# Kernel optimization log

Measured on AMD Instinct MI355X. Metric: run time of the kernel, lower is better.

## Reference

```python
import jax, jax.numpy as jnp
import numpy as np

TAU = 0.07
EPS = 1e-12  # F.normalize eps


def _l2norm(x):
    n = jnp.sqrt(jnp.sum(x * x, axis=-1, keepdims=True))
    return x / jnp.maximum(n, EPS)


def setup_inputs() -> dict:
    key = jax.random.key(0)
    k1, k2 = jax.random.split(key)
    n_e, e_dim = 4096, 64
    z = jax.random.normal(k1, (8, e_dim, 64, 64), dtype=jnp.float32)
    # embedding initialized uniform(-1/n_e, 1/n_e) in the module
    embedding = jax.random.uniform(k2, (n_e, e_dim), dtype=jnp.float32,
                                   minval=-1.0 / n_e, maxval=1.0 / n_e)
    return {"z": z, "embedding": embedding}


def reference(z, embedding):
    # z: [b, c, h, w] -> [b, h, w, c]
    b, c, h, w = z.shape
    z_bhwc = jnp.transpose(z.astype(jnp.float32), (0, 2, 3, 1))
    z_flat = _l2norm(z_bhwc.reshape(-1, c))          # [N, d]
    emb = _l2norm(embedding)                          # [n_e, d]
    logits = jnp.einsum('bd,nd->bn', z_flat, emb)     # [N, n_e]
    probs = jax.nn.softmax(logits / TAU, axis=-1)
    z_q_flat = probs @ emb                            # [N, d]
    z_q = _l2norm(z_q_flat.reshape(b, h, w, c))
    indices = jnp.argmax(probs, axis=-1)              # [N]
    entropy_loss = jnp.asarray(0.0, dtype=jnp.float32)  # eval mode
    z_q = jnp.transpose(z_q, (0, 3, 1, 2))            # back to [b, c, h, w]
    return (z_q, entropy_loss, indices)
```

## Files before the change

### kernel.cpp

```cpp
#include <hip/hip_runtime.h>
#include <hip/hip_bf16.h>

typedef unsigned short u16;
typedef unsigned int u32;
typedef __attribute__((ext_vector_type(4))) float f32x4;
typedef __attribute__((ext_vector_type(16))) float f32x16;
typedef __attribute__((ext_vector_type(4))) u32 u32x4;
typedef __attribute__((ext_vector_type(8))) __bf16 bf16x8;

#define LAM 20.60992915555662f

__device__ __forceinline__ void gl16(const void* g, void* l) {
  __builtin_amdgcn_global_load_lds(
      (const __attribute__((address_space(1))) unsigned int*)g,
      (__attribute__((address_space(3))) unsigned int*)l, 16, 0, 0);
}

__device__ __forceinline__ u32 cvtpk(float a, float b) {
  u32 r;
  asm("v_cvt_pk_bf16_f32 %0, %1, %2" : "=v"(r) : "v"(a), "v"(b));
  return r;
}

__device__ __forceinline__ float exp2a(float x) {
  float r;
  asm("v_exp_f32 %0, %1" : "=v"(r) : "v"(x));
  return r;
}

__global__ __launch_bounds__(256) void k_emb_prep(
    const float* __restrict__ emb, float* __restrict__ einv,
    u16* __restrict__ ehi, u16* __restrict__ elo, u16* __restrict__ et,
    float* __restrict__ out) {
  __shared__ u16 ehl[64][72];
  const int ch = blockIdx.x, t = threadIdx.x;
  const int e = t >> 2, q = t & 3;
  const int ge = ch * 64 + e;
  float v[16];
#pragma unroll
  for (int b = 0; b < 4; b++)
    *reinterpret_cast<float4*>(v + 4 * b) =
        *reinterpret_cast<const float4*>(emb + (size_t)ge * 64 + q * 16 + 4 * b);
  float ss = 0.f;
#pragma unroll
  for (int j = 0; j < 16; j++) ss += v[j] * v[j];
  ss += __shfl_xor(ss, 1);
  ss += __shfl_xor(ss, 2);
  float inv = 1.0f / fmaxf(sqrtf(ss), 1e-12f);
  if (q == 0) einv[ge] = inv;
  u16 hi[16], lo[16];
#pragma unroll
  for (int j = 0; j < 16; j++) {
    float n = v[j] * inv;
    __bf16 h = (__bf16)n;
    hi[j] = __builtin_bit_cast(u16, h);
    __bf16 l = (__bf16)(n - (float)h);
    lo[j] = __builtin_bit_cast(u16, l);
  }
#pragma unroll
  for (int bb = 0; bb < 2; bb++) {
    int b = 2 * q + bb;
    int pos = (b ^ (e & 7)) * 8;
    *reinterpret_cast<uint4*>(ehi + (size_t)ge * 64 + pos) =
        *reinterpret_cast<const uint4*>(hi + 8 * bb);
    *reinterpret_cast<uint4*>(elo + (size_t)ge * 64 + pos) =
        *reinterpret_cast<const uint4*>(lo + 8 * bb);
  }
  *reinterpret_cast<uint4*>(&ehl[e][q * 16]) = *reinterpret_cast<const uint4*>(hi);
  *reinterpret_cast<uint4*>(&ehl[e][q * 16 + 8]) = *reinterpret_cast<const uint4*>(hi + 8);
  __syncthreads();
  {
    const int d = t >> 2, eq = t & 3;
    u16 vals[16];
#pragma unroll
    for (int j = 0; j < 16; j++) vals[j] = ehl[eq * 16 + j][d];
#pragma unroll
    for (int bb = 0; bb < 2; bb++) {
      int b = 2 * eq + bb;
      int pos = (b ^ (d & 7)) * 8;
      *reinterpret_cast<uint4*>(et + (size_t)ch * 4096 + d * 64 + pos) =
          *reinterpret_cast<const uint4*>(vals + 8 * bb);
    }
  }
  if (ch == 0 && t == 0) out[2097152] = 0.0f;
}

__global__ __launch_bounds__(256) void k_z_prep(
    const float* __restrict__ z, u16* __restrict__ zhi, u16* __restrict__ zlo) {
  __shared__ float zt[64][65];
  int tid = threadIdx.x;
  int p0 = blockIdx.x * 64;
  const float* zb = z + (size_t)(p0 >> 12) * 262144 + (p0 & 4095);
#pragma unroll
  for (int k = 0; k < 4; k++) {
    int idx = k * 1024 + tid * 4;
    int c = idx >> 6, px = idx & 63;
    float4 v = *reinterpret_cast<const float4*>(zb + (size_t)c * 4096 + px);
    zt[c][px] = v.x; zt[c][px + 1] = v.y; zt[c][px + 2] = v.z; zt[c][px + 3] = v.w;
  }
  __syncthreads();
  int px = tid >> 2, cq = tid & 3;
  float ss = 0.f;
#pragma unroll
  for (int j = 0; j < 16; j++) { float v = zt[cq * 16 + j][px]; ss += v * v; }
  ss += __shfl_xor(ss, 1);
  ss += __shfl_xor(ss, 2);
  float inv = 1.0f / fmaxf(sqrtf(ss), 1e-12f);
  int p = p0 + px;
#pragma unroll
  for (int j0 = 0; j0 < 16; j0 += 4) {
    u16 hs[4], ls[4];
#pragma unroll
    for (int j = 0; j < 4; j++) {
      float n = zt[cq * 16 + j0 + j][px] * inv;
      __bf16 h = (__bf16)n;
      hs[j] = __builtin_bit_cast(u16, h);
      __bf16 l = (__bf16)(n - (float)h);
      ls[j] = __builtin_bit_cast(u16, l);
    }
    *reinterpret_cast<ushort4*>(zhi + (size_t)p * 64 + cq * 16 + j0) = make_ushort4(hs[0], hs[1], hs[2], hs[3]);
    *reinterpret_cast<ushort4*>(zlo + (size_t)p * 64 + cq * 16 + j0) = make_ushort4(ls[0], ls[1], ls[2], ls[3]);
  }
}

__global__ __launch_bounds__(256, 4) void k_main(
    const u16* __restrict__ zhi, const u16* __restrict__ zlo,
    const u16* __restrict__ ehi, const u16* __restrict__ elo,
    const u16* __restrict__ et, float* __restrict__ Osum,
    float* __restrict__ tv1, float* __restrict__ tv2, u32* __restrict__ tix) {
  __shared__ __align__(16) u16 sA[2][2][4096];
  __shared__ __align__(16) u16 sV[4096];
  const int t = threadIdx.x;
  const int w = t >> 6, lane = t & 63;
  const int H = lane >> 5, c = lane & 31;
  const int bx = blockIdx.x;
  const int s = bx >> 8, tile = bx & 255;
  const int px = tile * 128 + w * 32 + c;

  bf16x8 qh[4], ql[4];
#pragma unroll
  for (int kc = 0; kc < 4; kc++) {
    qh[kc] = *reinterpret_cast<const bf16x8*>(zhi + (size_t)px * 64 + kc * 16 + H * 8);
    ql[kc] = *reinterpret_cast<const bf16x8*>(zlo + (size_t)px * 64 + kc * 16 + H * 8);
  }

  int cb[4];
#pragma unroll
  for (int kc = 0; kc < 4; kc++) cb[kc] = 8 * ((2 * kc + H) ^ (c & 7));
  const int row0 = c * 64, row1 = (32 + c) * 64;

  f32x16 O0 = (f32x16)(0.0f), O1 = (f32x16)(0.0f);
  float v1 = -1e30f, v2 = -1e30f;
  int i1 = 0, i2 = 1;

  {
    const size_t gb = (size_t)(s * 16) * 4096;
#pragma unroll
    for (int u = 0; u < 2; u++) {
      int off = t * 8 + u * 2048;
      gl16(ehi + gb + off, &sA[0][0][off]);
      gl16(elo + gb + off, &sA[0][1][off]);
    }
  }
  __syncthreads();

  for (int ch = 0; ch < 16; ch++) {
    const int cur = ch & 1;
    {
      const size_t gv = (size_t)(s * 16 + ch) * 4096;
#pragma unroll
      for (int u = 0; u < 2; u++) {
        int off = t * 8 + u * 2048;
        gl16(et + gv + off, &sV[off]);
      }
    }
    if (ch + 1 < 16) {
      const size_t gb = (size_t)(s * 16 + ch + 1) * 4096;
#pragma unroll
      for (int u = 0; u < 2; u++) {
        int off = t * 8 + u * 2048;
        gl16(ehi + gb + off, &sA[cur ^ 1][0][off]);
        gl16(elo + gb + off, &sA[cur ^ 1][1][off]);
      }
    }
    const u16* sh = sA[cur][0];
    const u16* sl = sA[cur][1];

    f32x16 sa0, sa1;
    {
      f32x16 acc = (f32x16)(0.0f);
#pragma unroll
      for (int kc = 0; kc < 4; kc++) {
        bf16x8 ah = *reinterpret_cast<const bf16x8*>(&sh[row0 + cb[kc]]);
        bf16x8 al = *reinterpret_cast<const bf16x8*>(&sl[row0 + cb[kc]]);
        acc = __builtin_amdgcn_mfma_f32_32x32x16_bf16(ah, qh[kc], acc, 0, 0, 0);
        acc = __builtin_amdgcn_mfma_f32_32x32x16_bf16(al, qh[kc], acc, 0, 0, 0);
        acc = __builtin_amdgcn_mfma_f32_32x32x16_bf16(ah, ql[kc], acc, 0, 0, 0);
      }
      sa0 = acc;
    }
    {
      f32x16 acc = (f32x16)(0.0f);
#pragma unroll
      for (int kc = 0; kc < 4; kc++) {
        bf16x8 ah = *reinterpret_cast<const bf16x8*>(&sh[row1 + cb[kc]]);
        bf16x8 al = *reinterpret_cast<const bf16x8*>(&sl[row1 + cb[kc]]);
        acc = __builtin_amdgcn_mfma_f32_32x32x16_bf16(ah, qh[kc], acc, 0, 0, 0);
        acc = __builtin_amdgcn_mfma_f32_32x32x16_bf16(al, qh[kc], acc, 0, 0, 0);
        acc = __builtin_amdgcn_mfma_f32_32x32x16_bf16(ah, ql[kc], acc, 0, 0, 0);
      }
      sa1 = acc;
    }

    const int e0 = (s * 16 + ch) * 64;
    u32 pk[2][8], pko[2][8];
#pragma unroll
    for (int nt = 0; nt < 2; nt++) {
      float pe[16];
#pragma unroll
      for (int reg = 0; reg < 16; reg++) {
        float svv = nt ? sa1[reg] : sa0[reg];
        int eidx = e0 + nt * 32 + (reg & 3) + 8 * (reg >> 2) + 4 * H;
        if (svv > v1) { v2 = v1; i2 = i1; v1 = svv; i1 = eidx; }
        else if (svv > v2) { v2 = svv; i2 = eidx; }
        pe[reg] = exp2a(fmaf(svv, LAM, -LAM));
      }
#pragma unroll
      for (int qq = 0; qq < 8; qq++) pk[nt][qq] = cvtpk(pe[2 * qq], pe[2 * qq + 1]);
#pragma unroll
      for (int qq = 0; qq < 8; qq++) pko[nt][qq] = (u32)__shfl_xor((int)pk[nt][qq], 32);
    }

    __syncthreads();

#pragma unroll
    for (int km = 0; km < 4; km++) {
      const int nt = km >> 1, m1 = km & 1;
      u32x4 bv;
      bv.x = H ? pko[nt][(2 * m1 + 1) * 2 + 0] : pk[nt][(2 * m1) * 2 + 0];
      bv.y = H ? pko[nt][(2 * m1 + 1) * 2 + 1] : pk[nt][(2 * m1) * 2 + 1];
      bv.z = H ? pk[nt][(2 * m1 + 1) * 2 + 0] : pko[nt][(2 * m1) * 2 + 0];
      bv.w = H ? pk[nt][(2 * m1 + 1) * 2 + 1] : pko[nt][(2 * m1) * 2 + 1];
      bf16x8 pb = __builtin_bit_cast(bf16x8, bv);
      bf16x8 a0 = *reinterpret_cast<const bf16x8*>(&sV[row0 + cb[km]]);
      bf16x8 a1 = *reinterpret_cast<const bf16x8*>(&sV[row1 + cb[km]]);
      O0 = __builtin_amdgcn_mfma_f32_32x32x16_bf16(a0, pb, O0, 0, 0, 0);
      O1 = __builtin_amdgcn_mfma_f32_32x32x16_bf16(a1, pb, O1, 0, 0, 0);
    }
    __syncthreads();
  }

  {
    float o1 = __shfl_xor(v1, 32); int oi1 = __shfl_xor(i1, 32);
    float o2 = __shfl_xor(v2, 32); int oi2 = __shfl_xor(i2, 32);
    if (o1 > v1) { v2 = v1; i2 = i1; v1 = o1; i1 = oi1; }
    else if (o1 > v2) { v2 = o1; i2 = oi1; }
    if (o2 > v2) { v2 = o2; i2 = oi2; }
  }
  if (H == 0) {
    int o = s * 32768 + px;
    tv1[o] = v1;
    tv2[o] = v2;
    tix[o] = ((u32)i1 << 12) | (u32)i2;
  }
#pragma unroll
  for (int reg = 0; reg < 16; reg++) {
    int d0 = (reg & 3) + 8 * (reg >> 2) + 4 * H;
    unsafeAtomicAdd(&Osum[(size_t)d0 * 32768 + px], O0[reg]);
    unsafeAtomicAdd(&Osum[(size_t)(d0 + 32) * 32768 + px], O1[reg]);
  }
}

__global__ __launch_bounds__(256) void k_combine(
    const float* __restrict__ Osum, const float* __restrict__ tv1,
    const float* __restrict__ tv2, const u32* __restrict__ tix,
    const float* __restrict__ z, const float* __restrict__ emb,
    const float* __restrict__ einv, float* __restrict__ out) {
  const int t = threadIdx.x;
  const int px = blockIdx.x * 256 + t;
  const int b_ = px >> 12, hw = px & 4095;

  float ss = 0.f;
#pragma unroll 8
  for (int d = 0; d < 64; d++) {
    float v = Osum[(size_t)d * 32768 + px];
    ss = fmaf(v, v, ss);
  }
  float inv = 1.0f / fmaxf(sqrtf(ss), 1e-30f);
#pragma unroll 8
  for (int d = 0; d < 64; d++) {
    float v = Osum[(size_t)d * 32768 + px];
    out[(size_t)b_ * 262144 + (size_t)d * 4096 + hw] = v * inv;
  }

  float m1 = tv1[px], m2 = tv2[px];
  u32 ia = tix[px];
  int j1 = (int)(ia >> 12), j2 = (int)(ia & 0xFFF);
#pragma unroll
  for (int sg = 1; sg < 4; sg++) {
    float b1 = tv1[sg * 32768 + px], b2 = tv2[sg * 32768 + px];
    u32 ib = tix[sg * 32768 + px];
    int k1 = (int)(ib >> 12), k2 = (int)(ib & 0xFFF);
    if (b1 > m1) { m2 = m1; j2 = j1; m1 = b1; j1 = k1; }
    else if (b1 > m2) { m2 = b1; j2 = k1; }
    if (b2 > m2) { m2 = b2; j2 = k2; }
  }
  {
    const float* zc = z + (size_t)b_ * 262144 + hw;
    const float* e1 = emb + (size_t)j1 * 64;
    const float* e2 = emb + (size_t)j2 * 64;
    double d1 = 0.0, d2 = 0.0;
#pragma unroll 8
    for (int cc = 0; cc < 64; cc++) {
      double zv = (double)zc[(size_t)cc * 4096];
      d1 += zv * (double)e1[cc];
      d2 += zv * (double)e2[cc];
    }
    d1 *= (double)einv[j1];
    d2 *= (double)einv[j2];
    int best = (d2 > d1 || (d2 == d1 && j2 < j1)) ? j2 : j1;
    out[2097153 + px] = (float)best;
  }
}

extern "C" void kernel_launch(void* const* d_in, const int* in_sizes, int n_in,
                              void* d_out, int out_size, void* d_ws, size_t ws_size,
                              hipStream_t stream) {
  const float* z = (const float*)d_in[0];
  const float* emb = (const float*)d_in[1];
  float* out = (float*)d_out;
  char* ws = (char*)d_ws;
  float* Osum = (float*)(ws + 0);
  float* tv1  = (float*)(ws + 8388608);
  float* tv2  = (float*)(ws + 8912896);
  u32*   tix  = (u32*)(ws + 9437184);
  u16*   zhi  = (u16*)(ws + 9961472);
  u16*   zlo  = (u16*)(ws + 14155776);
  u16*   ehi  = (u16*)(ws + 18350080);
  u16*   elo  = (u16*)(ws + 18874368);
  u16*   et   = (u16*)(ws + 19398656);
  float* einv = (float*)(ws + 19922944);

  hipMemsetAsync(Osum, 0, 8388608, stream);
  k_emb_prep<<<dim3(64), dim3(256), 0, stream>>>(emb, einv, ehi, elo, et, out);
  k_z_prep<<<dim3(512), dim3(256), 0, stream>>>(z, zhi, zlo);
  k_main<<<dim3(1024), dim3(256), 0, stream>>>(zhi, zlo, ehi, elo, et, Osum, tv1, tv2, tix);
  k_combine<<<dim3(128), dim3(256), 0, stream>>>(Osum, tv1, tv2, tix, z, emb, einv, out);
}
```

Measured before the change: 180.9 us.

## Merge prep kernels, pack top-2 as integers, use permlane32 swap, widen combine

Fuses the embedding and z prep kernels into one launch that branches on block index. In the main kernel, the float top-2 tracking with index bookkeeping is replaced by packed fixed-point score|index u32 values updated with integer max/min. The cross-half shuffles used to assemble MFMA B operands are replaced by v_permlane32_swap. The combine kernel now gives four threads to each pixel, using 4x more blocks and shuffle reductions. The fixed-point quantization of scores (about 18 bits) can make near-ties order differently, though the fp64 recheck of the top two candidates reduces the effect on the final argmax.

```diff
diff --git a/kernel.cpp b/kernel.cpp
--- a/kernel.cpp
+++ b/kernel.cpp
@@ -28,98 +28,103 @@
   return r;
 }
 
-__global__ __launch_bounds__(256) void k_emb_prep(
-    const float* __restrict__ emb, float* __restrict__ einv,
-    u16* __restrict__ ehi, u16* __restrict__ elo, u16* __restrict__ et,
+__device__ __forceinline__ u32 umaxu(u32 a, u32 b) { return a > b ? a : b; }
+__device__ __forceinline__ u32 uminu(u32 a, u32 b) { return a < b ? a : b; }
+
+__global__ __launch_bounds__(256) void k_prep(
+    const float* __restrict__ emb, const float* __restrict__ z,
+    float* __restrict__ einv, u16* __restrict__ ehi, u16* __restrict__ elo,
+    u16* __restrict__ et, u16* __restrict__ zhi, u16* __restrict__ zlo,
     float* __restrict__ out) {
-  __shared__ u16 ehl[64][72];
-  const int ch = blockIdx.x, t = threadIdx.x;
-  const int e = t >> 2, q = t & 3;
-  const int ge = ch * 64 + e;
-  float v[16];
-#pragma unroll
-  for (int b = 0; b < 4; b++)
-    *reinterpret_cast<float4*>(v + 4 * b) =
-        *reinterpret_cast<const float4*>(emb + (size_t)ge * 64 + q * 16 + 4 * b);
-  float ss = 0.f;
-#pragma unroll
-  for (int j = 0; j < 16; j++) ss += v[j] * v[j];
-  ss += __shfl_xor(ss, 1);
-  ss += __shfl_xor(ss, 2);
-  float inv = 1.0f / fmaxf(sqrtf(ss), 1e-12f);
-  if (q == 0) einv[ge] = inv;
-  u16 hi[16], lo[16];
-#pragma unroll
-  for (int j = 0; j < 16; j++) {
-    float n = v[j] * inv;
-    __bf16 h = (__bf16)n;
-    hi[j] = __builtin_bit_cast(u16, h);
-    __bf16 l = (__bf16)(n - (float)h);
-    lo[j] = __builtin_bit_cast(u16, l);
-  }
-#pragma unroll
-  for (int bb = 0; bb < 2; bb++) {
-    int b = 2 * q + bb;
-    int pos = (b ^ (e & 7)) * 8;
-    *reinterpret_cast<uint4*>(ehi + (size_t)ge * 64 + pos) =
-        *reinterpret_cast<const uint4*>(hi + 8 * bb);
-    *reinterpret_cast<uint4*>(elo + (size_t)ge * 64 + pos) =
-        *reinterpret_cast<const uint4*>(lo + 8 * bb);
-  }
-  *reinterpret_cast<uint4*>(&ehl[e][q * 16]) = *reinterpret_cast<const uint4*>(hi);
-  *reinterpret_cast<uint4*>(&ehl[e][q * 16 + 8]) = *reinterpret_cast<const uint4*>(hi + 8);
-  __syncthreads();
-  {
-    const int d = t >> 2, eq = t & 3;
-    u16 vals[16];
-#pragma unroll
-    for (int j = 0; j < 16; j++) vals[j] = ehl[eq * 16 + j][d];
+  __shared__ union {
+    u16 ehl[64][72];
+    float zt[64][65];
+  } sm;
+  const int bx = blockIdx.x, t = threadIdx.x;
+  if (bx < 64) {
+    const int ch = bx;
+    const int e = t >> 2, q = t & 3;
+    const int ge = ch * 64 + e;
+    float v[16];
+#pragma unroll
+    for (int b = 0; b < 4; b++)
+      *reinterpret_cast<float4*>(v + 4 * b) =
+          *reinterpret_cast<const float4*>(emb + (size_t)ge * 64 + q * 16 + 4 * b);
+    float ss = 0.f;
+#pragma unroll
+    for (int j = 0; j < 16; j++) ss += v[j] * v[j];
+    ss += __shfl_xor(ss, 1);
+    ss += __shfl_xor(ss, 2);
+    float inv = 1.0f / fmaxf(sqrtf(ss), 1e-12f);
+    if (q == 0) einv[ge] = inv;
+    u16 hi[16], lo[16];
+#pragma unroll
+    for (int j = 0; j < 16; j++) {
+      float n = v[j] * inv;
+      __bf16 h = (__bf16)n;
+      hi[j] = __builtin_bit_cast(u16, h);
+      __bf16 l = (__bf16)(n - (float)h);
+      lo[j] = __builtin_bit_cast(u16, l);
+    }
 #pragma unroll
     for (int bb = 0; bb < 2; bb++) {
-      int b = 2 * eq + bb;
-      int pos = (b ^ (d & 7)) * 8;
-      *reinterpret_cast<uint4*>(et + (size_t)ch * 4096 + d * 64 + pos) =
-          *reinterpret_cast<const uint4*>(vals + 8 * bb);
-    }
-  }
-  if (ch == 0 && t == 0) out[2097152] = 0.0f;
-}
-
-__global__ __launch_bounds__(256) void k_z_prep(
-    const float* __restrict__ z, u16* __restrict__ zhi, u16* __restrict__ zlo) {
-  __shared__ float zt[64][65];
-  int tid = threadIdx.x;
-  int p0 = blockIdx.x * 64;
-  const float* zb = z + (size_t)(p0 >> 12) * 262144 + (p0 & 4095);
-#pragma unroll
-  for (int k = 0; k < 4; k++) {
-    int idx = k * 1024 + tid * 4;
-    int c = idx >> 6, px = idx & 63;
-    float4 v = *reinterpret_cast<const float4*>(zb + (size_t)c * 4096 + px);
-    zt[c][px] = v.x; zt[c][px + 1] = v.y; zt[c][px + 2] = v.z; zt[c][px + 3] = v.w;
-  }
-  __syncthreads();
-  int px = tid >> 2, cq = tid & 3;
-  float ss = 0.f;
-#pragma unroll
-  for (int j = 0; j < 16; j++) { float v = zt[cq * 16 + j][px]; ss += v * v; }
-  ss += __shfl_xor(ss, 1);
-  ss += __shfl_xor(ss, 2);
-  float inv = 1.0f / fmaxf(sqrtf(ss), 1e-12f);
-  int p = p0 + px;
-#pragma unroll
-  for (int j0 = 0; j0 < 16; j0 += 4) {
-    u16 hs[4], ls[4];
-#pragma unroll
-    for (int j = 0; j < 4; j++) {
-      float n = zt[cq * 16 + j0 + j][px] * inv;
-      __bf16 h = (__bf16)n;
-      hs[j] = __builtin_bit_cast(u16, h);
-      __bf16 l = (__bf16)(n - (float)h);
-      ls[j] = __builtin_bit_cast(u16, l);
-    }
-    *reinterpret_cast<ushort4*>(zhi + (size_t)p * 64 + cq * 16 + j0) = make_ushort4(hs[0], hs[1], hs[2], hs[3]);
-    *reinterpret_cast<ushort4*>(zlo + (size_t)p * 64 + cq * 16 + j0) = make_ushort4(ls[0], ls[1], ls[2], ls[3]);
+      int b = 2 * q + bb;
+      int pos = (b ^ (e & 7)) * 8;
+      *reinterpret_cast<uint4*>(ehi + (size_t)ge * 64 + pos) =
+          *reinterpret_cast<const uint4*>(hi + 8 * bb);
+      *reinterpret_cast<uint4*>(elo + (size_t)ge * 64 + pos) =
+          *reinterpret_cast<const uint4*>(lo + 8 * bb);
+    }
+    *reinterpret_cast<uint4*>(&sm.ehl[e][q * 16]) = *reinterpret_cast<const uint4*>(hi);
+    *reinterpret_cast<uint4*>(&sm.ehl[e][q * 16 + 8]) = *reinterpret_cast<const uint4*>(hi + 8);
+    __syncthreads();
+    {
+      const int d = t >> 2, eq = t & 3;
+      u16 vals[16];
+#pragma unroll
+      for (int j = 0; j < 16; j++) vals[j] = sm.ehl[eq * 16 + j][d];
+#pragma unroll
+      for (int bb = 0; bb < 2; bb++) {
+        int b = 2 * eq + bb;
+        int pos = (b ^ (d & 7)) * 8;
+        *reinterpret_cast<uint4*>(et + (size_t)ch * 4096 + d * 64 + pos) =
+            *reinterpret_cast<const uint4*>(vals + 8 * bb);
+      }
+    }
+    if (ch == 0 && t == 0) out[2097152] = 0.0f;
+  } else {
+    const int p0 = (bx - 64) * 64;
+    const float* zb = z + (size_t)(p0 >> 12) * 262144 + (p0 & 4095);
+#pragma unroll
+    for (int k = 0; k < 4; k++) {
+      int idx = k * 1024 + t * 4;
+      int c = idx >> 6, px = idx & 63;
+      float4 v = *reinterpret_cast<const float4*>(zb + (size_t)c * 4096 + px);
+      sm.zt[c][px] = v.x; sm.zt[c][px + 1] = v.y; sm.zt[c][px + 2] = v.z; sm.zt[c][px + 3] = v.w;
+    }
+    __syncthreads();
+    const int px = t >> 2, cq = t & 3;
+    float ss = 0.f;
+#pragma unroll
+    for (int j = 0; j < 16; j++) { float v = sm.zt[cq * 16 + j][px]; ss += v * v; }
+    ss += __shfl_xor(ss, 1);
+    ss += __shfl_xor(ss, 2);
+    float inv = 1.0f / fmaxf(sqrtf(ss), 1e-12f);
+    const int p = p0 + px;
+#pragma unroll
+    for (int j0 = 0; j0 < 16; j0 += 4) {
+      u16 hs[4], ls[4];
+#pragma unroll
+      for (int j = 0; j < 4; j++) {
+        float n = sm.zt[cq * 16 + j0 + j][px] * inv;
+        __bf16 h = (__bf16)n;
+        hs[j] = __builtin_bit_cast(u16, h);
+        __bf16 l = (__bf16)(n - (float)h);
+        ls[j] = __builtin_bit_cast(u16, l);
+      }
+      *reinterpret_cast<ushort4*>(zhi + (size_t)p * 64 + cq * 16 + j0) = make_ushort4(hs[0], hs[1], hs[2], hs[3]);
+      *reinterpret_cast<ushort4*>(zlo + (size_t)p * 64 + cq * 16 + j0) = make_ushort4(ls[0], ls[1], ls[2], ls[3]);
+    }
   }
 }
 
@@ -127,7 +132,7 @@
     const u16* __restrict__ zhi, const u16* __restrict__ zlo,
     const u16* __restrict__ ehi, const u16* __restrict__ elo,
     const u16* __restrict__ et, float* __restrict__ Osum,
-    float* __restrict__ tv1, float* __restrict__ tv2, u32* __restrict__ tix) {
+    u32* __restrict__ pk1, u32* __restrict__ pk2) {
   __shared__ __align__(16) u16 sA[2][2][4096];
   __shared__ __align__(16) u16 sV[4096];
   const int t = threadIdx.x;
@@ -150,8 +155,8 @@
   const int row0 = c * 64, row1 = (32 + c) * 64;
 
   f32x16 O0 = (f32x16)(0.0f), O1 = (f32x16)(0.0f);
-  float v1 = -1e30f, v2 = -1e30f;
-  int i1 = 0, i2 = 1;
+  u32 p1 = 0u, p2 = 0u;
+  const u32 vH4 = (u32)(4 * H);
 
   {
     const size_t gb = (size_t)(s * 16) * 4096;
@@ -213,22 +218,22 @@
     }
 
     const int e0 = (s * 16 + ch) * 64;
-    u32 pk[2][8], pko[2][8];
+    u32 pk[2][8];
 #pragma unroll
     for (int nt = 0; nt < 2; nt++) {
       float pe[16];
 #pragma unroll
       for (int reg = 0; reg < 16; reg++) {
         float svv = nt ? sa1[reg] : sa0[reg];
-        int eidx = e0 + nt * 32 + (reg & 3) + 8 * (reg >> 2) + 4 * H;
-        if (svv > v1) { v2 = v1; i2 = i1; v1 = svv; i1 = eidx; }
-        else if (svv > v2) { v2 = svv; i2 = eidx; }
+        u32 tfix = (u32)fmaf(svv, 262144.0f, 524288.0f);
+        u32 pckd = (tfix << 12) |
+                   ((u32)(e0 + nt * 32 + (reg & 3) + 8 * (reg >> 2)) | vH4);
+        p2 = umaxu(p2, uminu(pckd, p1));
+        p1 = umaxu(p1, pckd);
         pe[reg] = exp2a(fmaf(svv, LAM, -LAM));
       }
 #pragma unroll
       for (int qq = 0; qq < 8; qq++) pk[nt][qq] = cvtpk(pe[2 * qq], pe[2 * qq + 1]);
-#pragma unroll
-      for (int qq = 0; qq < 8; qq++) pko[nt][qq] = (u32)__shfl_xor((int)pk[nt][qq], 32);
     }
 
     __syncthreads();
@@ -236,11 +241,11 @@
 #pragma unroll
     for (int km = 0; km < 4; km++) {
       const int nt = km >> 1, m1 = km & 1;
-      u32x4 bv;
-      bv.x = H ? pko[nt][(2 * m1 + 1) * 2 + 0] : pk[nt][(2 * m1) * 2 + 0];
-      bv.y = H ? pko[nt][(2 * m1 + 1) * 2 + 1] : pk[nt][(2 * m1) * 2 + 1];
-      bv.z = H ? pk[nt][(2 * m1 + 1) * 2 + 0] : pko[nt][(2 * m1) * 2 + 0];
-      bv.w = H ? pk[nt][(2 * m1 + 1) * 2 + 1] : pko[nt][(2 * m1) * 2 + 1];
+      u32 ax = pk[nt][4 * m1 + 0], bx2 = pk[nt][4 * m1 + 2];
+      u32 ay = pk[nt][4 * m1 + 1], by2 = pk[nt][4 * m1 + 3];
+      asm("v_permlane32_swap_b32 %0, %1" : "+v"(ax), "+v"(bx2));
+      asm("v_permlane32_swap_b32 %0, %1" : "+v"(ay), "+v"(by2));
+      u32x4 bv; bv.x = ax; bv.y = ay; bv.z = bx2; bv.w = by2;
       bf16x8 pb = __builtin_bit_cast(bf16x8, bv);
       bf16x8 a0 = *reinterpret_cast<const bf16x8*>(&sV[row0 + cb[km]]);
       bf16x8 a1 = *reinterpret_cast<const bf16x8*>(&sV[row1 + cb[km]]);
@@ -251,17 +256,15 @@
   }
 
   {
-    float o1 = __shfl_xor(v1, 32); int oi1 = __shfl_xor(i1, 32);
-    float o2 = __shfl_xor(v2, 32); int oi2 = __shfl_xor(i2, 32);
-    if (o1 > v1) { v2 = v1; i2 = i1; v1 = o1; i1 = oi1; }
-    else if (o1 > v2) { v2 = o1; i2 = oi1; }
-    if (o2 > v2) { v2 = o2; i2 = oi2; }
-  }
-  if (H == 0) {
-    int o = s * 32768 + px;
-    tv1[o] = v1;
-    tv2[o] = v2;
-    tix[o] = ((u32)i1 << 12) | (u32)i2;
+    u32 o1 = (u32)__shfl_xor((int)p1, 32);
+    u32 o2 = (u32)__shfl_xor((int)p2, 32);
+    u32 n1 = umaxu(p1, o1);
+    u32 n2 = umaxu(uminu(p1, o1), umaxu(p2, o2));
+    if (H == 0) {
+      int o = s * 32768 + px;
+      pk1[o] = n1;
+      pk2[o] = n2;
+    }
   }
 #pragma unroll
   for (int reg = 0; reg < 16; reg++) {
@@ -272,54 +275,57 @@
 }
 
 __global__ __launch_bounds__(256) void k_combine(
-    const float* __restrict__ Osum, const float* __restrict__ tv1,
-    const float* __restrict__ tv2, const u32* __restrict__ tix,
-    const float* __restrict__ z, const float* __restrict__ emb,
-    const float* __restrict__ einv, float* __restrict__ out) {
+    const float* __restrict__ Osum, const u32* __restrict__ pk1,
+    const u32* __restrict__ pk2, const float* __restrict__ z,
+    const float* __restrict__ emb, const float* __restrict__ einv,
+    float* __restrict__ out) {
   const int t = threadIdx.x;
-  const int px = blockIdx.x * 256 + t;
+  const int pxl = t >> 2, part = t & 3;
+  const int px = blockIdx.x * 64 + pxl;
   const int b_ = px >> 12, hw = px & 4095;
 
+  float v[16];
+#pragma unroll
+  for (int j = 0; j < 16; j++) v[j] = Osum[(size_t)(part * 16 + j) * 32768 + px];
   float ss = 0.f;
-#pragma unroll 8
-  for (int d = 0; d < 64; d++) {
-    float v = Osum[(size_t)d * 32768 + px];
-    ss = fmaf(v, v, ss);
-  }
+#pragma unroll
+  for (int j = 0; j < 16; j++) ss = fmaf(v[j], v[j], ss);
+  ss += __shfl_xor(ss, 1);
+  ss += __shfl_xor(ss, 2);
   float inv = 1.0f / fmaxf(sqrtf(ss), 1e-30f);
-#pragma unroll 8
-  for (int d = 0; d < 64; d++) {
-    float v = Osum[(size_t)d * 32768 + px];
-    out[(size_t)b_ * 262144 + (size_t)d * 4096 + hw] = v * inv;
-  }
-
-  float m1 = tv1[px], m2 = tv2[px];
-  u32 ia = tix[px];
-  int j1 = (int)(ia >> 12), j2 = (int)(ia & 0xFFF);
+#pragma unroll
+  for (int j = 0; j < 16; j++)
+    out[(size_t)b_ * 262144 + (size_t)(part * 16 + j) * 4096 + hw] = v[j] * inv;
+
+  u32 m1 = pk1[px], m2 = pk2[px];
 #pragma unroll
   for (int sg = 1; sg < 4; sg++) {
-    float b1 = tv1[sg * 32768 + px], b2 = tv2[sg * 32768 + px];
-    u32 ib = tix[sg * 32768 + px];
-    int k1 = (int)(ib >> 12), k2 = (int)(ib & 0xFFF);
-    if (b1 > m1) { m2 = m1; j2 = j1; m1 = b1; j1 = k1; }
-    else if (b1 > m2) { m2 = b1; j2 = k1; }
-    if (b2 > m2) { m2 = b2; j2 = k2; }
-  }
+    u32 a1 = pk1[sg * 32768 + px], a2 = pk2[sg * 32768 + px];
+    u32 t2 = umaxu(umaxu(m2, a2), uminu(m1, a1));
+    m1 = umaxu(m1, a1);
+    m2 = t2;
+  }
+  const int j1 = (int)(m1 & 0xFFFu), j2 = (int)(m2 & 0xFFFu);
+
   {
-    const float* zc = z + (size_t)b_ * 262144 + hw;
-    const float* e1 = emb + (size_t)j1 * 64;
-    const float* e2 = emb + (size_t)j2 * 64;
+    const float* zc = z + (size_t)b_ * 262144 + (size_t)(part * 16) * 4096 + hw;
+    const float* e1 = emb + (size_t)j1 * 64 + part * 16;
+    const float* e2 = emb + (size_t)j2 * 64 + part * 16;
     double d1 = 0.0, d2 = 0.0;
-#pragma unroll 8
-    for (int cc = 0; cc < 64; cc++) {
-      double zv = (double)zc[(size_t)cc * 4096];
-      d1 += zv * (double)e1[cc];
-      d2 += zv * (double)e2[cc];
-    }
+#pragma unroll
+    for (int j = 0; j < 16; j++) {
+      double zv = (double)zc[(size_t)j * 4096];
+      d1 += zv * (double)e1[j];
+      d2 += zv * (double)e2[j];
+    }
+    d1 += __shfl_xor(d1, 1); d1 += __shfl_xor(d1, 2);
+    d2 += __shfl_xor(d2, 1); d2 += __shfl_xor(d2, 2);
     d1 *= (double)einv[j1];
     d2 *= (double)einv[j2];
-    int best = (d2 > d1 || (d2 == d1 && j2 < j1)) ? j2 : j1;
-    out[2097153 + px] = (float)best;
+    if (part == 0) {
+      int best = (d2 > d1 || (d2 == d1 && j2 < j1)) ? j2 : j1;
+      out[2097153 + px] = (float)best;
+    }
   }
 }
 
@@ -331,19 +337,17 @@
   float* out = (float*)d_out;
   char* ws = (char*)d_ws;
   float* Osum = (float*)(ws + 0);
-  float* tv1  = (float*)(ws + 8388608);
-  float* tv2  = (float*)(ws + 8912896);
-  u32*   tix  = (u32*)(ws + 9437184);
-  u16*   zhi  = (u16*)(ws + 9961472);
-  u16*   zlo  = (u16*)(ws + 14155776);
-  u16*   ehi  = (u16*)(ws + 18350080);
-  u16*   elo  = (u16*)(ws + 18874368);
-  u16*   et   = (u16*)(ws + 19398656);
-  float* einv = (float*)(ws + 19922944);
+  u32*   pk1  = (u32*)(ws + 8388608);
+  u32*   pk2  = (u32*)(ws + 8912896);
+  u16*   zhi  = (u16*)(ws + 9437184);
+  u16*   zlo  = (u16*)(ws + 13631488);
+  u16*   ehi  = (u16*)(ws + 17825792);
+  u16*   elo  = (u16*)(ws + 18350080);
+  u16*   et   = (u16*)(ws + 18874368);
+  float* einv = (float*)(ws + 19398656);
 
   hipMemsetAsync(Osum, 0, 8388608, stream);
-  k_emb_prep<<<dim3(64), dim3(256), 0, stream>>>(emb, einv, ehi, elo, et, out);
-  k_z_prep<<<dim3(512), dim3(256), 0, stream>>>(z, zhi, zlo);
-  k_main<<<dim3(1024), dim3(256), 0, stream>>>(zhi, zlo, ehi, elo, et, Osum, tv1, tv2, tix);
-  k_combine<<<dim3(128), dim3(256), 0, stream>>>(Osum, tv1, tv2, tix, z, emb, einv, out);
-}
+  k_prep<<<dim3(576), dim3(256), 0, stream>>>(emb, z, einv, ehi, elo, et, zhi, zlo, out);
+  k_main<<<dim3(1024), dim3(256), 0, stream>>>(zhi, zlo, ehi, elo, et, Osum, pk1, pk2);
+  k_combine<<<dim3(512), dim3(256), 0, stream>>>(Osum, pk1, pk2, z, emb, einv, out);
+}
```

New measurement: 170.2 us. 5.9% less time.
